# Kernel optimization log

Hardware: AMD Instinct MI355X
Metric: run time of the kernel (lower is better)

The kernel has to match this reference:

```python
import jax, jax.numpy as jnp
import numpy as np

MAX_TOKENS = 8192
MAX_NUM_NODES = 8192
FEATURES = 256


def setup_inputs() -> dict:
    key = jax.random.key(0)
    k_emb, k_start, k_end = jax.random.split(key, 3)
    embedding = jax.random.normal(k_emb, (MAX_NUM_NODES, FEATURES), dtype=jnp.float32)
    node_span_starts = jax.random.randint(k_start, (MAX_NUM_NODES,), 0, 4096, dtype=jnp.int32)
    node_span_ends = jax.random.randint(k_end, (MAX_NUM_NODES,), 0, MAX_TOKENS, dtype=jnp.int32)
    return {
        "embedding": embedding,
        "node_span_starts": node_span_starts,
        "node_span_ends": node_span_ends,
        "num_nodes": 6000,
    }


def reference(embedding, node_span_starts, node_span_ends, num_nodes):
    # For each token t: out[t] = sum over valid nodes n with start_n <= t <= end_n of embedding[n].
    # Identical math to the original vmap+where+sum, expressed as a masked matmul
    # to avoid the O(N*T*F) dense intermediate.
    t = jnp.arange(MAX_TOKENS)[:, None]                      # [T, 1]
    node_valid = jnp.arange(MAX_NUM_NODES) < num_nodes       # [N]
    in_span = (node_span_starts[None, :] <= t) & (t <= node_span_ends[None, :])  # [T, N]
    mask = (in_span & node_valid[None, :]).astype(embedding.dtype)               # [T, N]
    return mask @ embedding                                  # [T, F]
```

## Files before the change

kernel.cpp:

```cpp
#include <hip/hip_runtime.h>

#define T_TOKENS 8192
#define MAX_NODES 8192
#define FEAT 256
#define NCHUNKS 1024
#define CHUNK 8
#define NSUPER 32
#define SUPER 32
#define LIST_CAP 2048
#define EV_STRIDE LIST_CAP
#define QSCALE 65536.0f
#define QINV   (1.0f / 65536.0f)

#define APPLY_EVENT(eV, vV)                          \
    {                                                \
        const float sv_ = ((eV) & 1) ? -(vV) : (vV); \
        const int lr_ = ((eV) >> 1) & 7;             \
        d0 += (lr_ == 0) ? sv_ : 0.f;                \
        d1 += (lr_ == 1) ? sv_ : 0.f;                \
        d2 += (lr_ == 2) ? sv_ : 0.f;                \
        d3 += (lr_ == 3) ? sv_ : 0.f;                \
        d4 += (lr_ == 4) ? sv_ : 0.f;                \
        d5 += (lr_ == 5) ? sv_ : 0.f;                \
        d6 += (lr_ == 6) ? sv_ : 0.f;                \
        d7 += (lr_ == 7) ? sv_ : 0.f;                \
    }

__device__ __forceinline__ float sum_rows_plain(const float* __restrict__ p, int n, int f) {
    float r0 = 0.f, r1 = 0.f, r2 = 0.f, r3 = 0.f;
    float r4 = 0.f, r5 = 0.f, r6 = 0.f, r7 = 0.f;
    int i = 0;
    for (; i + 8 <= n; i += 8) {
        r0 += p[(size_t)(i + 0) * FEAT + f];
        r1 += p[(size_t)(i + 1) * FEAT + f];
        r2 += p[(size_t)(i + 2) * FEAT + f];
        r3 += p[(size_t)(i + 3) * FEAT + f];
        r4 += p[(size_t)(i + 4) * FEAT + f];
        r5 += p[(size_t)(i + 5) * FEAT + f];
        r6 += p[(size_t)(i + 6) * FEAT + f];
        r7 += p[(size_t)(i + 7) * FEAT + f];
    }
    for (; i < n; ++i) r0 += p[(size_t)i * FEAT + f];
    return ((r0 + r1) + (r2 + r3)) + ((r4 + r5) + (r6 + r7));
}

__device__ __forceinline__ float sum_qrows(const unsigned* __restrict__ p, int n, int f,
                                           unsigned P) {
    int r0 = 0, r1 = 0, r2 = 0, r3 = 0, r4 = 0, r5 = 0, r6 = 0, r7 = 0;
    int i = 0;
    for (; i + 8 <= n; i += 8) {
        r0 += (int)(p[(size_t)(i + 0) * FEAT + f] - P);
        r1 += (int)(p[(size_t)(i + 1) * FEAT + f] - P);
        r2 += (int)(p[(size_t)(i + 2) * FEAT + f] - P);
        r3 += (int)(p[(size_t)(i + 3) * FEAT + f] - P);
        r4 += (int)(p[(size_t)(i + 4) * FEAT + f] - P);
        r5 += (int)(p[(size_t)(i + 5) * FEAT + f] - P);
        r6 += (int)(p[(size_t)(i + 6) * FEAT + f] - P);
        r7 += (int)(p[(size_t)(i + 7) * FEAT + f] - P);
    }
    for (; i < n; ++i) r0 += (int)(p[(size_t)i * FEAT + f] - P);
    const int q = ((r0 + r1) + (r2 + r3)) + ((r4 + r5) + (r6 + r7));
    return (float)q * QINV;
}

__global__ __launch_bounds__(FEAT) void classify_kernel(
    const float* __restrict__ emb,
    const int* __restrict__ starts,
    const int* __restrict__ ends,
    const int* __restrict__ num_nodes_p,
    float* __restrict__ colsum,
    unsigned* __restrict__ supersum_q,
    int* __restrict__ evcnt,
    int* __restrict__ evbuf) {
    __shared__ int s_list[LIST_CAP];
    __shared__ int s_cnt;
    const int c = blockIdx.x;
    const int tid = threadIdx.x;
    const int f = tid;
    const int num_nodes = *num_nodes_p;
    const int row_lo = c * CHUNK;
    const int row_hi = row_lo + CHUNK;
    const int4* starts4 = (const int4*)starts;
    const int4* ends4 = (const int4*)ends;

    if (tid == 0) s_cnt = 0;
    __syncthreads();
#pragma unroll
    for (int r = 0; r < MAX_NODES / (4 * FEAT); ++r) {
        if (r * 4 * FEAT < num_nodes) {
            const int vec = r * FEAT + tid;
            const int4 s4 = starts4[vec];
            const int4 e4 = ends4[vec];
            const int sv[4] = {s4.x, s4.y, s4.z, s4.w};
            const int ev[4] = {e4.x, e4.y, e4.z, e4.w};
            const int nb = vec * 4;
#pragma unroll
            for (int k = 0; k < 4; ++k) {
                const int node = nb + k;
                const int s = sv[k];
                const int e = ev[k];
                if (node < num_nodes && s <= e && s < T_TOKENS && e >= 0) {
                    const int sc = s < 0 ? 0 : s;
                    if (sc >= row_lo && sc < row_hi) {
                        int p = atomicAdd(&s_cnt, 1);
                        if (p < LIST_CAP) s_list[p] = (node << 4) | ((sc - row_lo) << 1);
                    }
                    const int e1 = e + 1;
                    if (e1 < T_TOKENS && e1 >= row_lo && e1 < row_hi) {
                        int p = atomicAdd(&s_cnt, 1);
                        if (p < LIST_CAP) s_list[p] = (node << 4) | ((e1 - row_lo) << 1) | 1;
                    }
                }
            }
        }
    }
    __syncthreads();
    const int cnt = min(s_cnt, LIST_CAP);

    int* evb = evbuf + (size_t)c * EV_STRIDE;
    for (int j = tid; j < cnt; j += FEAT) evb[j] = s_list[j];
    if (tid == 0) evcnt[c] = cnt;

    float acc = 0.f;
    int j = 0;
    for (; j + 8 <= cnt; j += 8) {
        const int e0 = s_list[j + 0], e1 = s_list[j + 1];
        const int e2 = s_list[j + 2], e3 = s_list[j + 3];
        const int e4_ = s_list[j + 4], e5 = s_list[j + 5];
        const int e6 = s_list[j + 6], e7 = s_list[j + 7];
        const float v0 = emb[(size_t)(e0 >> 4) * FEAT + f];
        const float v1 = emb[(size_t)(e1 >> 4) * FEAT + f];
        const float v2 = emb[(size_t)(e2 >> 4) * FEAT + f];
        const float v3 = emb[(size_t)(e3 >> 4) * FEAT + f];
        const float v4 = emb[(size_t)(e4_ >> 4) * FEAT + f];
        const float v5 = emb[(size_t)(e5 >> 4) * FEAT + f];
        const float v6 = emb[(size_t)(e6 >> 4) * FEAT + f];
        const float v7 = emb[(size_t)(e7 >> 4) * FEAT + f];
        acc += (e0 & 1) ? -v0 : v0;
        acc += (e1 & 1) ? -v1 : v1;
        acc += (e2 & 1) ? -v2 : v2;
        acc += (e3 & 1) ? -v3 : v3;
        acc += (e4_ & 1) ? -v4 : v4;
        acc += (e5 & 1) ? -v5 : v5;
        acc += (e6 & 1) ? -v6 : v6;
        acc += (e7 & 1) ? -v7 : v7;
    }
    for (; j < cnt; ++j) {
        const int e0 = s_list[j];
        const float v0 = emb[(size_t)(e0 >> 4) * FEAT + f];
        acc += (e0 & 1) ? -v0 : v0;
    }
    colsum[(size_t)c * FEAT + f] = acc;

    const int q = __float2int_rn(acc * QSCALE);
    atomicAdd(&supersum_q[(size_t)(c >> 5) * FEAT + f], (unsigned)q);
}

__global__ __launch_bounds__(FEAT) void scan_kernel(
    const float* __restrict__ emb,
    const float* __restrict__ colsum,
    const unsigned* __restrict__ supersum_q,
    const unsigned* __restrict__ sentinel,
    const int* __restrict__ evcnt,
    const int* __restrict__ evbuf,
    float* __restrict__ out) {
    const int c = blockIdx.x;
    const int f = threadIdx.x;
    const int sg = c >> 5;

    const int cnt = evcnt[c];
    const int* evb = evbuf + (size_t)c * EV_STRIDE;

    const unsigned P = sentinel[f];
    float run = sum_qrows(supersum_q, sg, f, P) +
                sum_rows_plain(colsum + (size_t)sg * SUPER * FEAT, c & 31, f);

    float d0 = 0.f, d1 = 0.f, d2 = 0.f, d3 = 0.f;
    float d4 = 0.f, d5 = 0.f, d6 = 0.f, d7 = 0.f;
    int j = 0;
    for (; j + 4 <= cnt; j += 4) {
        const int e0 = evb[j + 0], e1 = evb[j + 1];
        const int e2 = evb[j + 2], e3 = evb[j + 3];
        const float v0 = emb[(size_t)(e0 >> 4) * FEAT + f];
        const float v1 = emb[(size_t)(e1 >> 4) * FEAT + f];
        const float v2 = emb[(size_t)(e2 >> 4) * FEAT + f];
        const float v3 = emb[(size_t)(e3 >> 4) * FEAT + f];
        APPLY_EVENT(e0, v0);
        APPLY_EVENT(e1, v1);
        APPLY_EVENT(e2, v2);
        APPLY_EVENT(e3, v3);
    }
    for (; j < cnt; ++j) {
        const int e0 = evb[j];
        const float v0 = emb[(size_t)(e0 >> 4) * FEAT + f];
        APPLY_EVENT(e0, v0);
    }

    float* o = out + (size_t)c * CHUNK * FEAT + f;
    run += d0; o[0 * FEAT] = run;
    run += d1; o[1 * FEAT] = run;
    run += d2; o[2 * FEAT] = run;
    run += d3; o[3 * FEAT] = run;
    run += d4; o[4 * FEAT] = run;
    run += d5; o[5 * FEAT] = run;
    run += d6; o[6 * FEAT] = run;
    run += d7; o[7 * FEAT] = run;
}

extern "C" void kernel_launch(void* const* d_in, const int* in_sizes, int n_in,
                              void* d_out, int out_size, void* d_ws, size_t ws_size,
                              hipStream_t stream) {
    (void)in_sizes; (void)n_in; (void)out_size; (void)ws_size;
    const float* emb     = (const float*)d_in[0];
    const int* starts    = (const int*)d_in[1];
    const int* ends      = (const int*)d_in[2];
    const int* num_nodes = (const int*)d_in[3];
    float* out           = (float*)d_out;

    unsigned* supersum_q = (unsigned*)d_ws;
    unsigned* sentinel   = supersum_q + (size_t)NSUPER * FEAT;
    float* colsum        = (float*)(sentinel + FEAT);
    int* evcnt           = (int*)(colsum + (size_t)NCHUNKS * FEAT);
    int* evbuf           = evcnt + NCHUNKS;

    classify_kernel<<<NCHUNKS, FEAT, 0, stream>>>(
        emb, starts, ends, num_nodes, colsum, supersum_q, evcnt, evbuf);
    scan_kernel<<<NCHUNKS, FEAT, 0, stream>>>(
        emb, colsum, supersum_q, sentinel, evcnt, evbuf, out);
}
```

Baseline: 82.05 us.

## Replace per-chunk redundant node scan with global atomic event scatter kernel

Previously each of the 1024 chunk blocks scanned every node to find the span events falling in its chunk, which repeats the same node scan once per block. A new scatter kernel assigns one thread per node and appends start and end events to the per-chunk lists with global atomics. Counters are read relative to a sentinel value from the workspace, and a separate colsum kernel then reads the events back from global memory. This removes the redundant scanning but adds a third launch, global atomic contention, and a nondeterministic event order within each chunk.

```diff
diff --git a/kernel.cpp b/kernel.cpp
--- a/kernel.cpp
+++ b/kernel.cpp
@@ -63,71 +63,61 @@
     return (float)q * QINV;
 }
 
-__global__ __launch_bounds__(FEAT) void classify_kernel(
-    const float* __restrict__ emb,
+__global__ __launch_bounds__(FEAT) void scatter_kernel(
     const int* __restrict__ starts,
     const int* __restrict__ ends,
     const int* __restrict__ num_nodes_p,
+    const unsigned* __restrict__ sentinel,
+    unsigned* __restrict__ evcnt_q,
+    int* __restrict__ evbuf) {
+    const int node = blockIdx.x * FEAT + threadIdx.x;
+    const int num_nodes = *num_nodes_p;
+    const unsigned P = sentinel[threadIdx.x];
+    if (node >= num_nodes) return;
+    const int s = starts[node];
+    const int e = ends[node];
+    if (s <= e && s < T_TOKENS && e >= 0) {
+        const int sc = s < 0 ? 0 : s;
+        {
+            const int chunk = sc >> 3;
+            const unsigned idx = atomicAdd(&evcnt_q[chunk], 1u) - P;
+            if (idx < LIST_CAP)
+                evbuf[(size_t)chunk * EV_STRIDE + idx] =
+                    (node << 4) | ((sc & 7) << 1);
+        }
+        const int e1 = e + 1;
+        if (e1 < T_TOKENS) {
+            const int chunk = e1 >> 3;
+            const unsigned idx = atomicAdd(&evcnt_q[chunk], 1u) - P;
+            if (idx < LIST_CAP)
+                evbuf[(size_t)chunk * EV_STRIDE + idx] =
+                    (node << 4) | ((e1 & 7) << 1) | 1;
+        }
+    }
+}
+
+__global__ __launch_bounds__(FEAT) void colsum_kernel(
+    const float* __restrict__ emb,
+    const unsigned* __restrict__ evcnt_q,
+    const int* __restrict__ evbuf,
+    const unsigned* __restrict__ sentinel,
     float* __restrict__ colsum,
-    unsigned* __restrict__ supersum_q,
-    int* __restrict__ evcnt,
-    int* __restrict__ evbuf) {
-    __shared__ int s_list[LIST_CAP];
-    __shared__ int s_cnt;
+    unsigned* __restrict__ supersum_q) {
     const int c = blockIdx.x;
-    const int tid = threadIdx.x;
-    const int f = tid;
-    const int num_nodes = *num_nodes_p;
-    const int row_lo = c * CHUNK;
-    const int row_hi = row_lo + CHUNK;
-    const int4* starts4 = (const int4*)starts;
-    const int4* ends4 = (const int4*)ends;
-
-    if (tid == 0) s_cnt = 0;
-    __syncthreads();
-#pragma unroll
-    for (int r = 0; r < MAX_NODES / (4 * FEAT); ++r) {
-        if (r * 4 * FEAT < num_nodes) {
-            const int vec = r * FEAT + tid;
-            const int4 s4 = starts4[vec];
-            const int4 e4 = ends4[vec];
-            const int sv[4] = {s4.x, s4.y, s4.z, s4.w};
-            const int ev[4] = {e4.x, e4.y, e4.z, e4.w};
-            const int nb = vec * 4;
-#pragma unroll
-            for (int k = 0; k < 4; ++k) {
-                const int node = nb + k;
-                const int s = sv[k];
-                const int e = ev[k];
-                if (node < num_nodes && s <= e && s < T_TOKENS && e >= 0) {
-                    const int sc = s < 0 ? 0 : s;
-                    if (sc >= row_lo && sc < row_hi) {
-                        int p = atomicAdd(&s_cnt, 1);
-                        if (p < LIST_CAP) s_list[p] = (node << 4) | ((sc - row_lo) << 1);
-                    }
-                    const int e1 = e + 1;
-                    if (e1 < T_TOKENS && e1 >= row_lo && e1 < row_hi) {
-                        int p = atomicAdd(&s_cnt, 1);
-                        if (p < LIST_CAP) s_list[p] = (node << 4) | ((e1 - row_lo) << 1) | 1;
-                    }
-                }
-            }
-        }
-    }
-    __syncthreads();
-    const int cnt = min(s_cnt, LIST_CAP);
-
-    int* evb = evbuf + (size_t)c * EV_STRIDE;
-    for (int j = tid; j < cnt; j += FEAT) evb[j] = s_list[j];
-    if (tid == 0) evcnt[c] = cnt;
+    const int f = threadIdx.x;
+    const unsigned P = sentinel[f];
+
+    const unsigned stored = evcnt_q[c];
+    const int cnt = min((int)(stored - P), LIST_CAP);
+    const int* evb = evbuf + (size_t)c * EV_STRIDE;
 
     float acc = 0.f;
     int j = 0;
     for (; j + 8 <= cnt; j += 8) {
-        const int e0 = s_list[j + 0], e1 = s_list[j + 1];
-        const int e2 = s_list[j + 2], e3 = s_list[j + 3];
-        const int e4_ = s_list[j + 4], e5 = s_list[j + 5];
-        const int e6 = s_list[j + 6], e7 = s_list[j + 7];
+        const int e0 = evb[j + 0], e1 = evb[j + 1];
+        const int e2 = evb[j + 2], e3 = evb[j + 3];
+        const int e4_ = evb[j + 4], e5 = evb[j + 5];
+        const int e6 = evb[j + 6], e7 = evb[j + 7];
         const float v0 = emb[(size_t)(e0 >> 4) * FEAT + f];
         const float v1 = emb[(size_t)(e1 >> 4) * FEAT + f];
         const float v2 = emb[(size_t)(e2 >> 4) * FEAT + f];
@@ -146,7 +136,7 @@
         acc += (e7 & 1) ? -v7 : v7;
     }
     for (; j < cnt; ++j) {
-        const int e0 = s_list[j];
+        const int e0 = evb[j];
         const float v0 = emb[(size_t)(e0 >> 4) * FEAT + f];
         acc += (e0 & 1) ? -v0 : v0;
     }
@@ -160,18 +150,18 @@
     const float* __restrict__ emb,
     const float* __restrict__ colsum,
     const unsigned* __restrict__ supersum_q,
+    const unsigned* __restrict__ evcnt_q,
     const unsigned* __restrict__ sentinel,
-    const int* __restrict__ evcnt,
     const int* __restrict__ evbuf,
     float* __restrict__ out) {
     const int c = blockIdx.x;
     const int f = threadIdx.x;
     const int sg = c >> 5;
 
-    const int cnt = evcnt[c];
+    const unsigned P = sentinel[f];
+    const int cnt = min((int)(evcnt_q[c] - P), LIST_CAP);
     const int* evb = evbuf + (size_t)c * EV_STRIDE;
 
-    const unsigned P = sentinel[f];
     float run = sum_qrows(supersum_q, sg, f, P) +
                 sum_rows_plain(colsum + (size_t)sg * SUPER * FEAT, c & 31, f);
 
@@ -217,14 +207,16 @@
     const int* num_nodes = (const int*)d_in[3];
     float* out           = (float*)d_out;
 
-    unsigned* supersum_q = (unsigned*)d_ws;
-    unsigned* sentinel   = supersum_q + (size_t)NSUPER * FEAT;
-    float* colsum        = (float*)(sentinel + FEAT);
-    int* evcnt           = (int*)(colsum + (size_t)NCHUNKS * FEAT);
-    int* evbuf           = evcnt + NCHUNKS;
-
-    classify_kernel<<<NCHUNKS, FEAT, 0, stream>>>(
-        emb, starts, ends, num_nodes, colsum, supersum_q, evcnt, evbuf);
+    unsigned* evcnt_q    = (unsigned*)d_ws;
+    unsigned* sentinel   = evcnt_q + NCHUNKS;
+    unsigned* supersum_q = sentinel + FEAT;
+    float* colsum        = (float*)(supersum_q + (size_t)NSUPER * FEAT);
+    int* evbuf           = (int*)(colsum + (size_t)NCHUNKS * FEAT);
+
+    scatter_kernel<<<MAX_NODES / FEAT, FEAT, 0, stream>>>(
+        starts, ends, num_nodes, sentinel, evcnt_q, evbuf);
+    colsum_kernel<<<NCHUNKS, FEAT, 0, stream>>>(
+        emb, evcnt_q, evbuf, sentinel, colsum, supersum_q);
     scan_kernel<<<NCHUNKS, FEAT, 0, stream>>>(
-        emb, colsum, supersum_q, sentinel, evcnt, evbuf, out);
-}
+        emb, colsum, supersum_q, evcnt_q, sentinel, evbuf, out);
+}
```

After: 81.45 us. No clear change (-0.7%).
